# Kernel tuning notes

Hardware: AMD Instinct MI355X
Metric: run time of the kernel (lower is better)

The kernel has to match this reference:

```python
import jax, jax.numpy as jnp
import numpy as np

K = 8           # neighbor_num
H = 8           # n_heads
DH = 64         # dim_single_head


def setup_inputs() -> dict:
    key = jax.random.key(0)
    ks = jax.random.split(key, 6)
    B, N, D = 2, 8192, 256
    inner = H * DH  # 512
    x = jax.random.normal(ks[0], (B, N, D), jnp.float32)
    center_pos3d = jax.random.normal(ks[1], (B, N, 3), jnp.float32)
    Wq = jax.random.normal(ks[2], (D, inner), jnp.float32) * 0.02
    Wkv = jax.random.normal(ks[3], (D, 2 * inner), jnp.float32) * 0.02
    Wout = jax.random.normal(ks[4], (inner, D), jnp.float32) * 0.02
    bout = jnp.zeros((D,), jnp.float32)
    return {"x": x, "center_pos3d": center_pos3d, "Wq": Wq, "Wkv": Wkv,
            "Wout": Wout, "bout": bout}


def _knn_idx(pos, k):
    # pos: [B,N,3] -> indices of k nearest neighbors per point, [B,N,k]
    sq = jnp.sum(pos * pos, axis=-1)                      # [B,N]
    d2 = sq[:, :, None] + sq[:, None, :] - 2.0 * jnp.einsum('bnc,bmc->bnm', pos, pos)
    _, idx = jax.lax.top_k(-d2, k)                        # smallest distances
    return idx


def reference(x, center_pos3d, Wq, Wkv, Wout, bout):
    B, N, D = x.shape
    inner = H * DH
    scale = DH ** -0.5

    idx = _knn_idx(center_pos3d, K)                       # [B,N,K] int32
    # grouping_operation: gather neighbor features -> [B,N,K,D]
    knn_x = jax.vmap(lambda xb, ib: xb[ib])(x, idx)

    q = (x @ Wq).reshape(B, N, H, DH)                     # [B,N,H,DH]
    kv = knn_x @ Wkv                                      # [B,N,K,2*inner]
    k_, v_ = jnp.split(kv, 2, axis=-1)
    k_ = k_.reshape(B, N, K, H, DH)
    v_ = v_.reshape(B, N, K, H, DH)

    dots = jnp.einsum('bnhd,bnkhd->bnhk', q, k_) * scale  # [B,N,H,K]
    attn = jax.nn.softmax(dots, axis=-1)
    out = jnp.einsum('bnhk,bnkhd->bnhd', attn, v_)        # [B,N,H,DH]
    out = out.reshape(B, N, inner)
    return out @ Wout + bout                              # dropout p=0 -> identity
```

## Files before the change

kernel.cpp:

```cpp
#include <hip/hip_runtime.h>
#include <hip/hip_bf16.h>

#define N_PTS 8192
#define KNN 8

typedef __attribute__((ext_vector_type(8))) short short8;
typedef __attribute__((ext_vector_type(4))) float float4v;
typedef unsigned long long u64;

static __device__ __forceinline__ short f2bf(float f) {
    unsigned u = __float_as_uint(f);
    unsigned r = (u + 0x7FFFu + ((u >> 16) & 1u)) >> 16;
    return (short)r;
}
static __device__ __forceinline__ float bf2f(short s) {
    return __uint_as_float(((unsigned)(unsigned short)s) << 16);
}

static __device__ __forceinline__ void ins8(u64* best, u64 x) {
#pragma unroll
    for (int j = 0; j < 8; ++j) {
        const u64 lo = x < best[j] ? x : best[j];
        const u64 hi = x < best[j] ? best[j] : x;
        best[j] = lo; x = hi;
    }
}

__global__ __launch_bounds__(256) void fused_knn_qkv(const float* __restrict__ pos,
                                                     u64* __restrict__ partial,
                                                     const short* __restrict__ A,
                                                     const short* __restrict__ Bt,
                                                     short* __restrict__ qall,
                                                     short* __restrict__ kvall)
{
    __shared__ char smem[40960];

    const int tid = threadIdx.x;
    const int g5 = blockIdx.x / 5;
    const int r5 = blockIdx.x % 5;

    if (r5 < 2) {
        const int kb = g5 * 2 + r5;
        float* sx = (float*)smem;
        float* sy = sx + 512;
        float* sz = sy + 512;
        u64* buf = (u64*)(smem + 6144);

        const int p   = kb & 15;
        const int qg  = kb >> 4;
        const int batch = qg >> 5;
        const int q_in_b = (qg & 31) * 256 + tid;
        const float* bpos = pos + (long)batch * N_PTS * 3;

        if (tid < 128) {
            const float* src = bpos + (p * 512 + tid * 4) * 3;
            const float4 f0 = *(const float4*)(src);
            const float4 f1 = *(const float4*)(src + 4);
            const float4 f2 = *(const float4*)(src + 8);
            const int c0 = tid * 4;
            *(float4*)&sx[c0] = make_float4(f0.x, f0.w, f1.z, f2.y);
            *(float4*)&sy[c0] = make_float4(f0.y, f1.x, f1.w, f2.z);
            *(float4*)&sz[c0] = make_float4(f0.z, f1.y, f2.x, f2.w);
        }
        __syncthreads();

        const float qx = bpos[q_in_b * 3 + 0];
        const float qy = bpos[q_in_b * 3 + 1];
        const float qz = bpos[q_in_b * 3 + 2];

        const float4* vx = (const float4*)sx;
        const float4* vy = (const float4*)sy;
        const float4* vz = (const float4*)sz;

        float bmin[32];
#pragma unroll
        for (int j = 0; j < 32; ++j) bmin[j] = 3.0e38f;

        for (int base = 0; base < 128; base += 8) {
#pragma unroll
            for (int g = 0; g < 8; ++g) {
                const float4 cx = vx[base + g];
                const float4 cy = vy[base + g];
                const float4 cz = vz[base + g];
                { const float dx = cx.x - qx, dy = cy.x - qy, dz = cz.x - qz;
                  bmin[g*4+0] = fminf(bmin[g*4+0], fmaf(dx, dx, fmaf(dy, dy, dz*dz))); }
                { const float dx = cx.y - qx, dy = cy.y - qy, dz = cz.y - qz;
                  bmin[g*4+1] = fminf(bmin[g*4+1], fmaf(dx, dx, fmaf(dy, dy, dz*dz))); }
                { const float dx = cx.z - qx, dy = cy.z - qy, dz = cz.z - qz;
                  bmin[g*4+2] = fminf(bmin[g*4+2], fmaf(dx, dx, fmaf(dy, dy, dz*dz))); }
                { const float dx = cx.w - qx, dy = cy.w - qy, dz = cz.w - qz;
                  bmin[g*4+3] = fminf(bmin[g*4+3], fmaf(dx, dx, fmaf(dy, dy, dz*dz))); }
            }
        }

        float t8[8];
#pragma unroll
        for (int j = 0; j < 8; ++j) t8[j] = 3.0e38f;
#pragma unroll
        for (int i = 0; i < 32; ++i) {
            float x = bmin[i];
#pragma unroll
            for (int j = 0; j < 8; ++j) {
                const float lo = fminf(t8[j], x);
                const float hi = fmaxf(t8[j], x);
                t8[j] = lo; x = hi;
            }
        }
        const float t = t8[7];

        int cnt = 0;
        for (int base = 0; base < 128; ++base) {
            const float4 cx = vx[base];
            const float4 cy = vy[base];
            const float4 cz = vz[base];
#pragma unroll
            for (int j = 0; j < 4; ++j) {
                const float ccx = j == 0 ? cx.x : j == 1 ? cx.y : j == 2 ? cx.z : cx.w;
                const float ccy = j == 0 ? cy.x : j == 1 ? cy.y : j == 2 ? cy.z : cy.w;
                const float ccz = j == 0 ? cz.x : j == 1 ? cz.y : j == 2 ? cz.z : cz.w;
                const float dx = ccx - qx, dy = ccy - qy, dz = ccz - qz;
                const float d2 = fmaf(dx, dx, fmaf(dy, dy, dz * dz));
                if (d2 <= t) {
                    buf[tid * 17 + (cnt < 16 ? cnt : 16)] =
                        ((u64)__float_as_uint(d2) << 32)
                        | (unsigned)(p * 512 + base * 4 + j);
                    ++cnt;
                }
            }
        }

        u64 best[8];
#pragma unroll
        for (int j = 0; j < 8; ++j) best[j] = ~0ULL;

        if (cnt <= 16) {
            for (int u = 0; u < cnt; ++u) ins8(best, buf[tid * 17 + u]);
        } else {
            for (int i = 0; i < 512; ++i) {
                const float dx = sx[i] - qx, dy = sy[i] - qy, dz = sz[i] - qz;
                const float d2 = fmaf(dx, dx, fmaf(dy, dy, dz * dz));
                u64 x = ((u64)__float_as_uint(d2) << 32) | (unsigned)(p * 512 + i);
                if (x < best[7]) ins8(best, x);
            }
        }

        const long qglob = (long)batch * N_PTS + q_in_b;
#pragma unroll
        for (int j = 0; j < 8; ++j)
            partial[(long)(p * 8 + j) * 16384 + qglob] = best[j];

    } else {
        const int id = g5 * 3 + (r5 - 2);
        const int bx = id % 12;
        const int by = id / 12;

        short (*As)[40] = (short(*)[40])smem;
        short (*Bs)[40] = (short(*)[40])(smem + 10240);

        const int lane = tid & 63;
        const int wv   = tid >> 6;
        const int quad = lane >> 4;
        const int l15  = lane & 15;
        const int m0 = by * 128;
        const int n0 = bx * 128;
        const int mh = (wv & 1) * 64, nh = (wv >> 1) * 64;

        const int srow  = tid >> 1;
        const int shalf = (tid & 1) * 16;
        const int Kd = 256;

        float4v acc[4][4];
#pragma unroll
        for (int i = 0; i < 4; ++i)
#pragma unroll
            for (int j = 0; j < 4; ++j) acc[i][j] = (float4v)(0.f);

        for (int k0 = 0; k0 < Kd; k0 += 32) {
            const short8* asrc = (const short8*)(A + (long)(m0 + srow) * Kd + k0 + shalf);
            const short8* bsrc = (const short8*)(Bt + (long)(n0 + srow) * Kd + k0 + shalf);
            *(short8*)&As[srow][shalf]     = asrc[0];
            *(short8*)&As[srow][shalf + 8] = asrc[1];
            *(short8*)&Bs[srow][shalf]     = bsrc[0];
            *(short8*)&Bs[srow][shalf + 8] = bsrc[1];
            __syncthreads();

            short8 af[4], bfv[4];
#pragma unroll
            for (int i = 0; i < 4; ++i)
                af[i] = *(const short8*)&As[mh + i * 16 + l15][quad * 8];
#pragma unroll
            for (int j = 0; j < 4; ++j)
                bfv[j] = *(const short8*)&Bs[nh + j * 16 + l15][quad * 8];
#pragma unroll
            for (int i = 0; i < 4; ++i)
#pragma unroll
                for (int j = 0; j < 4; ++j)
                    acc[i][j] = __builtin_amdgcn_mfma_f32_16x16x32_bf16(af[i], bfv[j], acc[i][j], 0, 0, 0);
            __syncthreads();
        }

        short* Cb;
        int stride, cb;
        if (n0 < 512) { Cb = qall;  stride = 512;  cb = n0; }
        else          { Cb = kvall; stride = 1024; cb = n0 - 512; }

#pragma unroll
        for (int i = 0; i < 4; ++i)
#pragma unroll
            for (int j = 0; j < 4; ++j) {
                const int col = cb + nh + j * 16 + l15;
#pragma unroll
                for (int r = 0; r < 4; ++r) {
                    const int row = m0 + mh + i * 16 + quad * 4 + r;
                    Cb[(long)row * stride + col] = f2bf(acc[i][j][r]);
                }
            }
    }
}

__global__ __launch_bounds__(256) void knn_merge(const u64* __restrict__ partial,
                                                 int* __restrict__ idxo)
{
    const int q = blockIdx.x * 256 + threadIdx.x;
    u64 best[8];
#pragma unroll
    for (int j = 0; j < 8; ++j) best[j] = ~0ULL;
    for (int s = 0; s < 128; ++s) {
        u64 x = partial[(long)s * 16384 + q];
        if (x < best[7]) ins8(best, x);
    }
#pragma unroll
    for (int j = 0; j < 8; ++j)
        idxo[(long)q * 8 + j] = (int)(best[j] & 0xFFFFFFFFu);
}

__global__ __launch_bounds__(256) void conv_all(const float* __restrict__ x,
                                                const float* __restrict__ Wq,
                                                const float* __restrict__ Wkv,
                                                const float* __restrict__ Wout,
                                                short* __restrict__ xb,
                                                short* __restrict__ wqkvt,
                                                short* __restrict__ woutt)
{
    const int bid = blockIdx.x;
    const int tid = threadIdx.x;
    if (bid < 2048) {
        const int i = bid * 256 + tid;
        const float4 a = ((const float4*)x)[i * 2];
        const float4 b = ((const float4*)x)[i * 2 + 1];
        short8 w = {f2bf(a.x), f2bf(a.y), f2bf(a.z), f2bf(a.w),
                    f2bf(b.x), f2bf(b.y), f2bf(b.z), f2bf(b.w)};
        ((short8*)xb)[i] = w;
    } else if (bid < 2560) {
        const int o = (bid - 2048) * 256 + tid;
        const int n = o >> 8, k = o & 255;
        wqkvt[o] = f2bf(Wq[(long)k * 512 + n]);
    } else if (bid < 3584) {
        const int o = (bid - 2560) * 256 + tid;
        const int n = o >> 8, k = o & 255;
        wqkvt[131072 + o] = f2bf(Wkv[(long)k * 1024 + n]);
    } else {
        const int o = (bid - 3584) * 256 + tid;
        const int n = o >> 9, k = o & 511;
        woutt[o] = f2bf(Wout[(long)k * 256 + n]);
    }
}

__global__ __launch_bounds__(256) void gemm_out(const short* __restrict__ A,
                                                const short* __restrict__ Bt,
                                                const float* __restrict__ bias,
                                                float* __restrict__ C,
                                                int N, int Kd)
{
    __shared__ short As[128][40];
    __shared__ short Bs[128][40];

    const int tid  = threadIdx.x;
    const int lane = tid & 63;
    const int wv   = tid >> 6;
    const int quad = lane >> 4;
    const int l15  = lane & 15;
    const int m0 = blockIdx.y * 128;
    const int n0 = blockIdx.x * 128;
    const int mh = (wv & 1) * 64, nh = (wv >> 1) * 64;

    const int srow  = tid >> 1;
    const int shalf = (tid & 1) * 16;

    float4v acc[4][4];
#pragma unroll
    for (int i = 0; i < 4; ++i)
#pragma unroll
        for (int j = 0; j < 4; ++j) acc[i][j] = (float4v)(0.f);

    for (int k0 = 0; k0 < Kd; k0 += 32) {
        const short8* asrc = (const short8*)(A + (long)(m0 + srow) * Kd + k0 + shalf);
        const short8* bsrc = (const short8*)(Bt + (long)(n0 + srow) * Kd + k0 + shalf);
        *(short8*)&As[srow][shalf]     = asrc[0];
        *(short8*)&As[srow][shalf + 8] = asrc[1];
        *(short8*)&Bs[srow][shalf]     = bsrc[0];
        *(short8*)&Bs[srow][shalf + 8] = bsrc[1];
        __syncthreads();

        short8 af[4], bfv[4];
#pragma unroll
        for (int i = 0; i < 4; ++i)
            af[i] = *(const short8*)&As[mh + i * 16 + l15][quad * 8];
#pragma unroll
        for (int j = 0; j < 4; ++j)
            bfv[j] = *(const short8*)&Bs[nh + j * 16 + l15][quad * 8];
#pragma unroll
        for (int i = 0; i < 4; ++i)
#pragma unroll
            for (int j = 0; j < 4; ++j)
                acc[i][j] = __builtin_amdgcn_mfma_f32_16x16x32_bf16(af[i], bfv[j], acc[i][j], 0, 0, 0);
        __syncthreads();
    }

#pragma unroll
    for (int i = 0; i < 4; ++i)
#pragma unroll
        for (int j = 0; j < 4; ++j) {
            const int col = n0 + nh + j * 16 + l15;
            const float bb = bias[col];
#pragma unroll
            for (int r = 0; r < 4; ++r) {
                const int row = m0 + mh + i * 16 + quad * 4 + r;
                C[(long)row * N + col] = acc[i][j][r] + bb;
            }
        }
}

__global__ __launch_bounds__(256) void attn_kernel(const short* qall,
                                                   const short* __restrict__ kvall,
                                                   const int* __restrict__ idxp,
                                                   short* outp)
{
    __shared__ float attn_s[4][8][8];
    const int wave = threadIdx.x >> 6;
    const int lane = threadIdx.x & 63;
    const int g = blockIdx.x * 4 + wave;
    const int b = g >> 13;
    const int* myidx = idxp + (long)g * 8;

    {
        const int h = lane >> 3;
        const int k = lane & 7;
        const int j = myidx[k];
        const short8* qrow = (const short8*)(qall + (long)g * 512 + h * 64);
        const short8* krow = (const short8*)(kvall + ((long)(b * N_PTS + j)) * 1024 + h * 64);

        float dot = 0.f;
#pragma unroll
        for (int c = 0; c < 8; ++c) {
            const short8 qv = qrow[c];
            const short8 kv = krow[c];
#pragma unroll
            for (int e = 0; e < 8; ++e)
                dot = fmaf(bf2f(qv[e]), bf2f(kv[e]), dot);
        }
        dot *= 0.125f;

        float m = dot;
#pragma unroll
        for (int off = 1; off < 8; off <<= 1)
            m = fmaxf(m, __shfl_xor(m, off, 8));
        const float e = __expf(dot - m);
        float ssum = e;
#pragma unroll
        for (int off = 1; off < 8; off <<= 1)
            ssum += __shfl_xor(ssum, off, 8);
        attn_s[wave][h][k] = e / ssum;
    }
    __syncthreads();

    const int d8 = lane * 8;
    const int h2 = lane >> 3;
    float o[8] = {0.f, 0.f, 0.f, 0.f, 0.f, 0.f, 0.f, 0.f};
#pragma unroll
    for (int kk = 0; kk < 8; ++kk) {
        const int jj = myidx[kk];
        const float w = attn_s[wave][h2][kk];
        const short8 v = *(const short8*)(kvall + ((long)(b * N_PTS + jj)) * 1024 + 512 + d8);
#pragma unroll
        for (int e = 0; e < 8; ++e)
            o[e] = fmaf(w, bf2f(v[e]), o[e]);
    }
    short8 ov = {f2bf(o[0]), f2bf(o[1]), f2bf(o[2]), f2bf(o[3]),
                 f2bf(o[4]), f2bf(o[5]), f2bf(o[6]), f2bf(o[7])};
    *(short8*)(outp + (long)g * 512 + d8) = ov;
}

extern "C" void kernel_launch(void* const* d_in, const int* in_sizes, int n_in,
                              void* d_out, int out_size, void* d_ws, size_t ws_size,
                              hipStream_t stream)
{
    const float* x    = (const float*)d_in[0];
    const float* pos  = (const float*)d_in[1];
    const float* Wq   = (const float*)d_in[2];
    const float* Wkv  = (const float*)d_in[3];
    const float* Wout = (const float*)d_in[4];
    const float* bout = (const float*)d_in[5];
    float* out = (float*)d_out;

    const int M = 16384;

    char* ws = (char*)d_ws;
    int*   idxp  = (int*)ws;                          ws += 1 << 19;
    short* qall  = (short*)ws;                        ws += (long)M * 512 * 2;
    short* kvall = (short*)ws;                        ws += (long)M * 1024 * 2;
    short* xb    = (short*)ws;                        ws += (long)M * 256 * 2;
    short* wqkvt = (short*)ws;                        ws += 1536 * 256 * 2;
    short* woutt = (short*)ws;                        ws += 256 * 512 * 2;
    u64*  partial = (u64*)ws;                         ws += (long)128 * 16384 * 8;

    conv_all<<<4096, 256, 0, stream>>>(x, Wq, Wkv, Wout, xb, wqkvt, woutt);
    fused_knn_qkv<<<2560, 256, 0, stream>>>(pos, partial, xb, wqkvt, qall, kvall);
    knn_merge<<<64, 256, 0, stream>>>(partial, idxp);
    attn_kernel<<<M / 4, 256, 0, stream>>>(qall, kvall, idxp, qall);
    gemm_out<<<dim3(2, 128), 256, 0, stream>>>(qall, woutt, bout, out, 256, 512);
}
```

Measured before the change: 323.1 us.

## Regroup kernels: overlap KNN with bf16 conversion, merge with QKV GEMM

Re-pairs the co-scheduled work across kernels. KNN partial blocks now share a launch with the fp32-to-bf16 conversion (interleaved 1:4), and the KNN merge shares a launch with the QKV GEMM (64 merge blocks plus 1536 GEMM blocks). This removes the standalone conversion and merge launches. The aim is to hide the short, latency-bound merge and conversion work under heavier compute and cut a launch, at the cost of a new interleaving ratio that may balance the memory-bound and compute-bound blocks differently.

```diff
diff --git a/kernel.cpp b/kernel.cpp
--- a/kernel.cpp
+++ b/kernel.cpp
@@ -26,21 +26,23 @@
     }
 }
 
-__global__ __launch_bounds__(256) void fused_knn_qkv(const float* __restrict__ pos,
-                                                     u64* __restrict__ partial,
-                                                     const short* __restrict__ A,
-                                                     const short* __restrict__ Bt,
-                                                     short* __restrict__ qall,
-                                                     short* __restrict__ kvall)
+__global__ __launch_bounds__(256) void fused_knn_conv(const float* __restrict__ pos,
+                                                      u64* __restrict__ partial,
+                                                      const float* __restrict__ x,
+                                                      const float* __restrict__ Wq,
+                                                      const float* __restrict__ Wkv,
+                                                      const float* __restrict__ Wout,
+                                                      short* __restrict__ xb,
+                                                      short* __restrict__ wqkvt,
+                                                      short* __restrict__ woutt)
 {
     __shared__ char smem[40960];
-
     const int tid = threadIdx.x;
     const int g5 = blockIdx.x / 5;
     const int r5 = blockIdx.x % 5;
 
-    if (r5 < 2) {
-        const int kb = g5 * 2 + r5;
+    if (r5 == 0) {
+        const int kb = g5;
         float* sx = (float*)smem;
         float* sy = sx + 512;
         float* sz = sy + 512;
@@ -98,12 +100,12 @@
         for (int j = 0; j < 8; ++j) t8[j] = 3.0e38f;
 #pragma unroll
         for (int i = 0; i < 32; ++i) {
-            float x = bmin[i];
+            float x_ = bmin[i];
 #pragma unroll
             for (int j = 0; j < 8; ++j) {
-                const float lo = fminf(t8[j], x);
-                const float hi = fmaxf(t8[j], x);
-                t8[j] = lo; x = hi;
+                const float lo = fminf(t8[j], x_);
+                const float hi = fmaxf(t8[j], x_);
+                t8[j] = lo; x_ = hi;
             }
         }
         const float t = t8[7];
@@ -139,8 +141,8 @@
             for (int i = 0; i < 512; ++i) {
                 const float dx = sx[i] - qx, dy = sy[i] - qy, dz = sz[i] - qz;
                 const float d2 = fmaf(dx, dx, fmaf(dy, dy, dz * dz));
-                u64 x = ((u64)__float_as_uint(d2) << 32) | (unsigned)(p * 512 + i);
-                if (x < best[7]) ins8(best, x);
+                u64 x_ = ((u64)__float_as_uint(d2) << 32) | (unsigned)(p * 512 + i);
+                if (x_ < best[7]) ins8(best, x_);
             }
         }
 
@@ -150,142 +152,72 @@
             partial[(long)(p * 8 + j) * 16384 + qglob] = best[j];
 
     } else {
-        const int id = g5 * 3 + (r5 - 2);
-        const int bx = id % 12;
-        const int by = id / 12;
-
-        short (*As)[40] = (short(*)[40])smem;
-        short (*Bs)[40] = (short(*)[40])(smem + 10240);
-
-        const int lane = tid & 63;
-        const int wv   = tid >> 6;
-        const int quad = lane >> 4;
-        const int l15  = lane & 15;
-        const int m0 = by * 128;
-        const int n0 = bx * 128;
-        const int mh = (wv & 1) * 64, nh = (wv >> 1) * 64;
-
-        const int srow  = tid >> 1;
-        const int shalf = (tid & 1) * 16;
-        const int Kd = 256;
-
-        float4v acc[4][4];
-#pragma unroll
-        for (int i = 0; i < 4; ++i)
-#pragma unroll
-            for (int j = 0; j < 4; ++j) acc[i][j] = (float4v)(0.f);
-
-        for (int k0 = 0; k0 < Kd; k0 += 32) {
-            const short8* asrc = (const short8*)(A + (long)(m0 + srow) * Kd + k0 + shalf);
-            const short8* bsrc = (const short8*)(Bt + (long)(n0 + srow) * Kd + k0 + shalf);
-            *(short8*)&As[srow][shalf]     = asrc[0];
-            *(short8*)&As[srow][shalf + 8] = asrc[1];
-            *(short8*)&Bs[srow][shalf]     = bsrc[0];
-            *(short8*)&Bs[srow][shalf + 8] = bsrc[1];
-            __syncthreads();
-
-            short8 af[4], bfv[4];
-#pragma unroll
-            for (int i = 0; i < 4; ++i)
-                af[i] = *(const short8*)&As[mh + i * 16 + l15][quad * 8];
-#pragma unroll
-            for (int j = 0; j < 4; ++j)
-                bfv[j] = *(const short8*)&Bs[nh + j * 16 + l15][quad * 8];
-#pragma unroll
-            for (int i = 0; i < 4; ++i)
-#pragma unroll
-                for (int j = 0; j < 4; ++j)
-                    acc[i][j] = __builtin_amdgcn_mfma_f32_16x16x32_bf16(af[i], bfv[j], acc[i][j], 0, 0, 0);
-            __syncthreads();
-        }
-
-        short* Cb;
-        int stride, cb;
-        if (n0 < 512) { Cb = qall;  stride = 512;  cb = n0; }
-        else          { Cb = kvall; stride = 1024; cb = n0 - 512; }
-
-#pragma unroll
-        for (int i = 0; i < 4; ++i)
-#pragma unroll
-            for (int j = 0; j < 4; ++j) {
-                const int col = cb + nh + j * 16 + l15;
-#pragma unroll
-                for (int r = 0; r < 4; ++r) {
-                    const int row = m0 + mh + i * 16 + quad * 4 + r;
-                    Cb[(long)row * stride + col] = f2bf(acc[i][j][r]);
-                }
-            }
-    }
-}
-
-__global__ __launch_bounds__(256) void knn_merge(const u64* __restrict__ partial,
-                                                 int* __restrict__ idxo)
-{
-    const int q = blockIdx.x * 256 + threadIdx.x;
-    u64 best[8];
-#pragma unroll
-    for (int j = 0; j < 8; ++j) best[j] = ~0ULL;
-    for (int s = 0; s < 128; ++s) {
-        u64 x = partial[(long)s * 16384 + q];
-        if (x < best[7]) ins8(best, x);
-    }
-#pragma unroll
-    for (int j = 0; j < 8; ++j)
-        idxo[(long)q * 8 + j] = (int)(best[j] & 0xFFFFFFFFu);
-}
-
-__global__ __launch_bounds__(256) void conv_all(const float* __restrict__ x,
-                                                const float* __restrict__ Wq,
-                                                const float* __restrict__ Wkv,
-                                                const float* __restrict__ Wout,
-                                                short* __restrict__ xb,
-                                                short* __restrict__ wqkvt,
-                                                short* __restrict__ woutt)
-{
-    const int bid = blockIdx.x;
-    const int tid = threadIdx.x;
-    if (bid < 2048) {
-        const int i = bid * 256 + tid;
-        const float4 a = ((const float4*)x)[i * 2];
-        const float4 b = ((const float4*)x)[i * 2 + 1];
-        short8 w = {f2bf(a.x), f2bf(a.y), f2bf(a.z), f2bf(a.w),
-                    f2bf(b.x), f2bf(b.y), f2bf(b.z), f2bf(b.w)};
-        ((short8*)xb)[i] = w;
-    } else if (bid < 2560) {
-        const int o = (bid - 2048) * 256 + tid;
-        const int n = o >> 8, k = o & 255;
-        wqkvt[o] = f2bf(Wq[(long)k * 512 + n]);
-    } else if (bid < 3584) {
-        const int o = (bid - 2560) * 256 + tid;
-        const int n = o >> 8, k = o & 255;
-        wqkvt[131072 + o] = f2bf(Wkv[(long)k * 1024 + n]);
-    } else {
-        const int o = (bid - 3584) * 256 + tid;
-        const int n = o >> 9, k = o & 511;
-        woutt[o] = f2bf(Wout[(long)k * 256 + n]);
-    }
-}
-
-__global__ __launch_bounds__(256) void gemm_out(const short* __restrict__ A,
-                                                const short* __restrict__ Bt,
-                                                const float* __restrict__ bias,
-                                                float* __restrict__ C,
-                                                int N, int Kd)
+        const int bid = g5 * 4 + (r5 - 1);
+        if (bid < 2048) {
+            const int i = bid * 256 + tid;
+            const float4 a = ((const float4*)x)[i * 2];
+            const float4 b = ((const float4*)x)[i * 2 + 1];
+            short8 w = {f2bf(a.x), f2bf(a.y), f2bf(a.z), f2bf(a.w),
+                        f2bf(b.x), f2bf(b.y), f2bf(b.z), f2bf(b.w)};
+            ((short8*)xb)[i] = w;
+        } else if (bid < 2560) {
+            const int o = (bid - 2048) * 256 + tid;
+            const int n = o >> 8, k = o & 255;
+            wqkvt[o] = f2bf(Wq[(long)k * 512 + n]);
+        } else if (bid < 3584) {
+            const int o = (bid - 2560) * 256 + tid;
+            const int n = o >> 8, k = o & 255;
+            wqkvt[131072 + o] = f2bf(Wkv[(long)k * 1024 + n]);
+        } else {
+            const int o = (bid - 3584) * 256 + tid;
+            const int n = o >> 9, k = o & 511;
+            woutt[o] = f2bf(Wout[(long)k * 256 + n]);
+        }
+    }
+}
+
+__global__ __launch_bounds__(256) void fused_gemm_merge(const short* __restrict__ A,
+                                                        const short* __restrict__ Bt,
+                                                        short* __restrict__ qall,
+                                                        short* __restrict__ kvall,
+                                                        const u64* __restrict__ partial,
+                                                        int* __restrict__ idxo)
 {
     __shared__ short As[128][40];
     __shared__ short Bs[128][40];
 
-    const int tid  = threadIdx.x;
+    const int tid = threadIdx.x;
+
+    if (blockIdx.x < 64) {
+        const int q = blockIdx.x * 256 + tid;
+        u64 best[8];
+#pragma unroll
+        for (int j = 0; j < 8; ++j) best[j] = ~0ULL;
+        for (int s = 0; s < 128; ++s) {
+            u64 x = partial[(long)s * 16384 + q];
+            if (x < best[7]) ins8(best, x);
+        }
+#pragma unroll
+        for (int j = 0; j < 8; ++j)
+            idxo[(long)q * 8 + j] = (int)(best[j] & 0xFFFFFFFFu);
+        return;
+    }
+
+    const int id = blockIdx.x - 64;
+    const int bx = id % 12;
+    const int by = id / 12;
+
     const int lane = tid & 63;
     const int wv   = tid >> 6;
     const int quad = lane >> 4;
     const int l15  = lane & 15;
-    const int m0 = blockIdx.y * 128;
-    const int n0 = blockIdx.x * 128;
+    const int m0 = by * 128;
+    const int n0 = bx * 128;
     const int mh = (wv & 1) * 64, nh = (wv >> 1) * 64;
 
     const int srow  = tid >> 1;
     const int shalf = (tid & 1) * 16;
+    const int Kd = 256;
 
     float4v acc[4][4];
 #pragma unroll
@@ -317,16 +249,20 @@
         __syncthreads();
     }
 
+    short* Cb;
+    int stride, cb;
+    if (n0 < 512) { Cb = qall;  stride = 512;  cb = n0; }
+    else          { Cb = kvall; stride = 1024; cb = n0 - 512; }
+
 #pragma unroll
     for (int i = 0; i < 4; ++i)
 #pragma unroll
         for (int j = 0; j < 4; ++j) {
-            const int col = n0 + nh + j * 16 + l15;
-            const float bb = bias[col];
+            const int col = cb + nh + j * 16 + l15;
 #pragma unroll
             for (int r = 0; r < 4; ++r) {
                 const int row = m0 + mh + i * 16 + quad * 4 + r;
-                C[(long)row * N + col] = acc[i][j][r] + bb;
+                Cb[(long)row * stride + col] = f2bf(acc[i][j][r]);
             }
         }
 }
@@ -391,6 +327,71 @@
     *(short8*)(outp + (long)g * 512 + d8) = ov;
 }
 
+__global__ __launch_bounds__(256) void gemm_out(const short* __restrict__ A,
+                                                const short* __restrict__ Bt,
+                                                const float* __restrict__ bias,
+                                                float* __restrict__ C,
+                                                int N, int Kd)
+{
+    __shared__ short As[128][40];
+    __shared__ short Bs[128][40];
+
+    const int tid  = threadIdx.x;
+    const int lane = tid & 63;
+    const int wv   = tid >> 6;
+    const int quad = lane >> 4;
+    const int l15  = lane & 15;
+    const int m0 = blockIdx.y * 128;
+    const int n0 = blockIdx.x * 128;
+    const int mh = (wv & 1) * 64, nh = (wv >> 1) * 64;
+
+    const int srow  = tid >> 1;
+    const int shalf = (tid & 1) * 16;
+
+    float4v acc[4][4];
+#pragma unroll
+    for (int i = 0; i < 4; ++i)
+#pragma unroll
+        for (int j = 0; j < 4; ++j) acc[i][j] = (float4v)(0.f);
+
+    for (int k0 = 0; k0 < Kd; k0 += 32) {
+        const short8* asrc = (const short8*)(A + (long)(m0 + srow) * Kd + k0 + shalf);
+        const short8* bsrc = (const short8*)(Bt + (long)(n0 + srow) * Kd + k0 + shalf);
+        *(short8*)&As[srow][shalf]     = asrc[0];
+        *(short8*)&As[srow][shalf + 8] = asrc[1];
+        *(short8*)&Bs[srow][shalf]     = bsrc[0];
+        *(short8*)&Bs[srow][shalf + 8] = bsrc[1];
+        __syncthreads();
+
+        short8 af[4], bfv[4];
+#pragma unroll
+        for (int i = 0; i < 4; ++i)
+            af[i] = *(const short8*)&As[mh + i * 16 + l15][quad * 8];
+#pragma unroll
+        for (int j = 0; j < 4; ++j)
+            bfv[j] = *(const short8*)&Bs[nh + j * 16 + l15][quad * 8];
+#pragma unroll
+        for (int i = 0; i < 4; ++i)
+#pragma unroll
+            for (int j = 0; j < 4; ++j)
+                acc[i][j] = __builtin_amdgcn_mfma_f32_16x16x32_bf16(af[i], bfv[j], acc[i][j], 0, 0, 0);
+        __syncthreads();
+    }
+
+#pragma unroll
+    for (int i = 0; i < 4; ++i)
+#pragma unroll
+        for (int j = 0; j < 4; ++j) {
+            const int col = n0 + nh + j * 16 + l15;
+            const float bb = bias[col];
+#pragma unroll
+            for (int r = 0; r < 4; ++r) {
+                const int row = m0 + mh + i * 16 + quad * 4 + r;
+                C[(long)row * N + col] = acc[i][j][r] + bb;
+            }
+        }
+}
+
 extern "C" void kernel_launch(void* const* d_in, const int* in_sizes, int n_in,
                               void* d_out, int out_size, void* d_ws, size_t ws_size,
                               hipStream_t stream)
@@ -414,9 +415,9 @@
     short* woutt = (short*)ws;                        ws += 256 * 512 * 2;
     u64*  partial = (u64*)ws;                         ws += (long)128 * 16384 * 8;
 
-    conv_all<<<4096, 256, 0, stream>>>(x, Wq, Wkv, Wout, xb, wqkvt, woutt);
-    fused_knn_qkv<<<2560, 256, 0, stream>>>(pos, partial, xb, wqkvt, qall, kvall);
-    knn_merge<<<64, 256, 0, stream>>>(partial, idxp);
+    fused_knn_conv<<<5120, 256, 0, stream>>>(pos, partial, x, Wq, Wkv, Wout,
+                                             xb, wqkvt, woutt);
+    fused_gemm_merge<<<1600, 256, 0, stream>>>(xb, wqkvt, qall, kvall, partial, idxp);
     attn_kernel<<<M / 4, 256, 0, stream>>>(qall, kvall, idxp, qall);
     gemm_out<<<dim3(2, 128), 256, 0, stream>>>(qall, woutt, bout, out, 256, 512);
 }
```

Result: faster. 301.1 us (-6.8%).
